# Kernel optimization log

Measured on AMD Instinct MI355X. Metric: run time of the kernel, lower is better.

## Reference

```python
import jax, jax.numpy as jnp
import numpy as np

B, C, H, W = 2, 96, 128, 128
G, NH, KH, KW = 12, 12, 3, 3
K = KH * KW
Cg = C // G          # 8 channels per deformable group
HD = C // NH         # 8 dims per head
MLP = int(2.0 * C)


def _conv3x3(x, w, b):
    y = jax.lax.conv_general_dilated(x, w, (1, 1), 'SAME',
                                     dimension_numbers=('NCHW', 'OIHW', 'NCHW'))
    return y + b[None, :, None, None]


def _prelu(x, a):
    return jnp.where(x >= 0, x, a[None, :, None, None] * x)


def _bilinear(img_flat, xs, ys, h, w):
    # img_flat: [N, C, H*W]; xs, ys: [N, P] pixel coords. Zero padding outside.
    x0 = jnp.floor(xs)
    y0 = jnp.floor(ys)
    wx = xs - x0
    wy = ys - y0

    def gather(xi, yi, wt):
        valid = ((xi >= 0) & (xi < w) & (yi >= 0) & (yi < h)).astype(img_flat.dtype)
        xc = jnp.clip(xi, 0, w - 1).astype(jnp.int32)
        yc = jnp.clip(yi, 0, h - 1).astype(jnp.int32)
        v = jnp.take_along_axis(img_flat, (yc * w + xc)[:, None, :], axis=2)
        return v * (wt * valid)[:, None, :]

    return (gather(x0, y0, (1 - wx) * (1 - wy)) + gather(x0 + 1, y0, wx * (1 - wy))
            + gather(x0, y0 + 1, (1 - wx) * wy) + gather(x0 + 1, y0 + 1, wx * wy))


def setup_inputs() -> dict:
    key = jax.random.key(0)
    ks = jax.random.split(key, 24)

    def n(k, shape, s):
        return jax.random.normal(k, shape, jnp.float32) * s

    d = {
        'feat_t': jax.random.normal(ks[0], (B, C, H, W), jnp.float32),
        'feat_kv': jax.random.normal(ks[1], (B, C, H, W), jnp.float32),
        'flow': jax.random.normal(ks[2], (B, 2, H, W), jnp.float32),
        # offset-prediction convs (zero-init in source; small random to exercise math)
        'cw1': n(ks[3], (2 * C, 2 * C + 2, 3, 3), 0.02), 'cb1': jnp.zeros((2 * C,), jnp.float32),
        'a1': jnp.full((2 * C,), 0.25, jnp.float32),
        'cw2': n(ks[4], (C, 2 * C, 3, 3), 0.02), 'cb2': jnp.zeros((C,), jnp.float32),
        'a2': jnp.full((C,), 0.25, jnp.float32),
        'cw3': n(ks[5], (G * K * 2, C, 3, 3), 0.01), 'cb3': jnp.zeros((G * K * 2,), jnp.float32),
        # attention projections
        'wq': n(ks[6], (C, C), C ** -0.5), 'bq': jnp.zeros((C,), jnp.float32),
        'wk': n(ks[7], (C, C), C ** -0.5), 'bk': jnp.zeros((C,), jnp.float32),
        'wv': n(ks[8], (C, C), C ** -0.5), 'bv': jnp.zeros((C,), jnp.float32),
        'wo': n(ks[9], (C, C), C ** -0.5), 'bo': jnp.zeros((C,), jnp.float32),
        # MLP (mlp_ratio = 2.0)
        'wm1': n(ks[10], (MLP, C), C ** -0.5), 'bm1': jnp.zeros((MLP,), jnp.float32),
        'wm2': n(ks[11], (C, MLP), MLP ** -0.5), 'bm2': jnp.zeros((C,), jnp.float32),
    }
    return d


def reference(feat_t, feat_kv, flow, cw1, cb1, a1, cw2, cb2, a2, cw3, cb3,
              wq, bq, wk, bk, wv, bv, wo, bo, wm1, bm1, wm2, bm2):
    b, c, h, w = feat_t.shape
    P = h * w
    dt = feat_t.dtype
    gy, gx = jnp.meshgrid(jnp.arange(h, dtype=dt), jnp.arange(w, dtype=dt), indexing='ij')

    # 1) backward-warp kv features to the query frame (flow channels = (x, y))
    xs = (gx[None] + flow[:, 0]).reshape(b, P)
    ys = (gy[None] + flow[:, 1]).reshape(b, P)
    kv_to_q = _bilinear(feat_kv.reshape(b, c, P), xs, ys, h, w).reshape(b, c, h, w)

    # 2) residual offsets from conv stack; add flow (flipped to (y, x)) tiled G*K times
    r = _prelu(_conv3x3(jnp.concatenate([feat_t, kv_to_q, flow], axis=1), cw1, cb1), a1)
    r = _prelu(_conv3x3(r, cw2, cb2), a2)
    r = _conv3x3(r, cw3, cb3)                                  # [B, G*K*2, H, W]
    offset = r + jnp.tile(flow[:, ::-1], (1, G * K, 1, 1))
    off = offset.reshape(b, G, K, 2, h, w)                     # [..., (dy, dx), H, W]

    # 3) grouped deformable bilinear sampling over the 3x3 window
    wy_, wx_ = jnp.meshgrid(jnp.arange(KH, dtype=dt) - (KH - 1) / 2,
                            jnp.arange(KW, dtype=dt) - (KW - 1) / 2, indexing='ij')
    win_y = wy_.reshape(K)
    win_x = wx_.reshape(K)
    sx = gx[None, None, None] + win_x[None, None, :, None, None] + off[:, :, :, 1]
    sy = gy[None, None, None] + win_y[None, None, :, None, None] + off[:, :, :, 0]
    img_g = feat_kv.reshape(b * G, Cg, P)
    samp = _bilinear(img_g, sx.reshape(b * G, K * P), sy.reshape(b * G, K * P), h, w)
    kv = samp.reshape(b, G, Cg, K, h, w).reshape(b, c, K, h, w)  # [B, C, K, H, W]

    # 4) multi-head attention: each query pixel attends over its K sampled points
    q = jnp.einsum('oc,bchw->bohw', wq, feat_t) + bq[None, :, None, None]
    k = jnp.einsum('oc,bckhw->bokhw', wk, kv) + bk[None, :, None, None, None]
    v = jnp.einsum('oc,bckhw->bokhw', wv, kv) + bv[None, :, None, None, None]
    qh = q.reshape(b, NH, HD, P)
    kh = k.reshape(b, NH, HD, K, P)
    vh = v.reshape(b, NH, HD, K, P)
    scale = 1.0 / np.sqrt(HD).astype(np.float32)
    attn = jax.nn.softmax(jnp.einsum('bhdp,bhdkp->bhkp', qh, kh) * scale, axis=2)
    o = jnp.einsum('bhkp,bhdkp->bhdp', attn, vh).reshape(b, c, h, w)
    x = feat_t + jnp.einsum('oc,bchw->bohw', wo, o) + bo[None, :, None, None]

    # 5) MLP (ratio 2.0) with residual
    hdn = jax.nn.gelu(jnp.einsum('oc,bchw->bohw', wm1, x) + bm1[None, :, None, None])
    return x + jnp.einsum('oc,bchw->bohw', wm2, hdn) + bm2[None, :, None, None]
```

## Files before the change

### kernel.cpp

```cpp
#include <hip/hip_runtime.h>
#include <hip/hip_bf16.h>
#include <math.h>

typedef __hip_bfloat16 bf16;
typedef __attribute__((ext_vector_type(8))) short s16x8;
typedef __attribute__((ext_vector_type(4))) short s16x4;
typedef __attribute__((ext_vector_type(4))) float fx4;
typedef __attribute__((ext_vector_type(2))) float f32x2;

#define Bv 2
#define Cv 96
#define Hv 128
#define Wv 128
#define Pv (Hv*Wv)
#define NPIX (Bv*Pv)
#define Gv 12
#define Kv 9
#define PPB 7
#define NPT 64
#define SROW 104
#define KROW 200

__device__ __forceinline__ float b2f(bf16 x) { return __bfloat162float(x); }
__device__ __forceinline__ bf16 f2b(float x) { return __float2bfloat16(x); }

__device__ __forceinline__ void gld16(const void* g, void* l) {
    __builtin_amdgcn_global_load_lds(
        (const __attribute__((address_space(1))) unsigned int*)g,
        (__attribute__((address_space(3))) unsigned int*)l, 16, 0, 0);
}

__device__ __forceinline__ float ldin(const void* p, size_t i, int isf) {
    return isf ? ((const float*)p)[i] : __bfloat162float(((const bf16*)p)[i]);
}

__device__ __forceinline__ void acc_pk(f32x2 acc[4], uint4 d, float wt) {
    f32x2 w2; w2.x = wt; w2.y = wt;
    #pragma unroll
    for (int q = 0; q < 4; q++) {
        unsigned u = (&d.x)[q];
        f32x2 v;
        v.x = __uint_as_float(u << 16);
        v.y = __uint_as_float(u & 0xffff0000u);
        acc[q] += w2 * v;
    }
}

__device__ __forceinline__ s16x8 pack8(const f32x2 a[4]) {
    s16x8 st;
    #pragma unroll
    for (int q = 0; q < 4; q++) {
        bf16 l = f2b(a[q].x), h = f2b(a[q].y);
        st[q*2]   = *(short*)&l;
        st[q*2+1] = *(short*)&h;
    }
    return st;
}

__global__ void detect_dtype(const unsigned short* __restrict__ x, int* __restrict__ flag,
                             float* __restrict__ zbuf)
{
    __shared__ int bad;
    if (threadIdx.x == 0) bad = 0;
    if (threadIdx.x < 64) zbuf[threadIdx.x] = 0.f;
    __syncthreads();
    int cnt = 0;
    for (int i = threadIdx.x; i < 32768; i += 256) {
        unsigned short u = x[i];
        if ((u & 0x7F80) == 0x7F80) cnt++;
    }
    atomicAdd(&bad, cnt);
    __syncthreads();
    if (threadIdx.x == 0) flag[0] = (bad > 0) ? 1 : 0;
}

__global__ void transpose_feats(const int* __restrict__ flag,
                                const void* ft, const void* fkv,
                                bf16* __restrict__ cat, bf16* __restrict__ fkvclb)
{
    __shared__ short tft[64*104];
    __shared__ short tkv[64*104];
    int tid = threadIdx.x;
    int isf = flag[0];
    int gp0 = blockIdx.x * 64;
    int bb  = gp0 >> 14;
    int p0  = gp0 & (Pv-1);

    for (int e = tid; e < 96*64; e += 256) {
        int c = e >> 6, dp = e & 63;
        size_t gi = ((size_t)bb*96 + c)*Pv + p0 + dp;
        bf16 v1 = f2b(ldin(ft,  gi, isf));
        bf16 v2 = f2b(ldin(fkv, gi, isf));
        tft[dp*104 + c] = *(short*)&v1;
        tkv[dp*104 + c] = *(short*)&v2;
    }
    __syncthreads();

    for (int u = tid; u < 64*12; u += 256) {
        int g = u % 12, px = u / 12;
        s16x8 a = *(const s16x8*)&tft[px*104 + g*8];
        s16x8 b = *(const s16x8*)&tkv[px*104 + g*8];
        *(s16x8*)(cat    + (size_t)(gp0+px)*224 + g*8) = a;
        *(s16x8*)(fkvclb + (size_t)(gp0+px)*96  + g*8) = b;
    }
}

__global__ void prep_weights(const int* __restrict__ flag,
    const void* flow,
    const void* cw1, const void* cb1, const void* a1,
    const void* cw2, const void* cb2, const void* a2,
    const void* cw3, const void* cb3,
    const void* wq, const void* bq, const void* wk, const void* bk,
    const void* wv, const void* bv, const void* wo, const void* bo,
    const void* wm1, const void* bm1, const void* wm2, const void* bm2,
    float* __restrict__ flowf,
    bf16* __restrict__ wAq, bf16* __restrict__ wAo, bf16* __restrict__ wAkv,
    bf16* __restrict__ wA1, bf16* __restrict__ wA2, bf16* __restrict__ wA3,
    bf16* __restrict__ wAm1, bf16* __restrict__ wAm2,
    float* __restrict__ biasf)
{
    int isf = flag[0];
    size_t i = (size_t)blockIdx.x * 256 + threadIdx.x;
    if (i < (size_t)Bv*2*Pv) flowf[i] = ldin(flow, i, isf);

    if (i < 9*7*192*32) {
        int q = (int)(i & 31);
        int rest = (int)(i >> 5);
        int co = rest % 192; rest /= 192;
        int kc = rest % 7;   int t = rest / 7;
        int ci = kc*32 + q;
        float v = (ci < 194) ? ldin(cw1, (size_t)co*194*9 + (size_t)ci*9 + t, isf) : 0.f;
        wA1[i] = f2b(v);
    }
    if (i < 9*6*96*32) {
        int q = (int)(i & 31);
        int rest = (int)(i >> 5);
        int co = rest % 96; rest /= 96;
        int kc = rest % 6;  int t = rest / 6;
        int ci = kc*32 + q;
        wA2[i] = f2b(ldin(cw2, (size_t)co*192*9 + (size_t)ci*9 + t, isf));
    }
    if (i < 9*3*256*32) {
        int q = (int)(i & 31);
        int rest = (int)(i >> 5);
        int co = rest % 256; rest /= 256;
        int kc = rest % 3;   int t = rest / 3;
        int ci = kc*32 + q;
        float v = (co < 216) ? ldin(cw3, (size_t)co*96*9 + (size_t)ci*9 + t, isf) : 0.f;
        wA3[i] = f2b(v);
    }
    if (i < 3*192*32) {
        int q = (int)(i & 31);
        int rest = (int)(i >> 5);
        int co = rest % 192;
        int kc = rest / 192;
        wAm1[i] = f2b(ldin(wm1, (size_t)co*96 + kc*32 + q, isf));
    }
    if (i < 6*96*32) {
        int q = (int)(i & 31);
        int rest = (int)(i >> 5);
        int co = rest % 96;
        int kc = rest / 96;
        wAm2[i] = f2b(ldin(wm2, (size_t)co*192 + kc*32 + q, isf));
    }
    if (i < 3*96*32) {
        int q = (int)(i & 31);
        int rest = (int)(i >> 5);
        int co = rest % 96;
        int kc = rest / 96;
        wAq[i] = f2b(ldin(wq, (size_t)co*96 + kc*32 + q, isf));
        wAo[i] = f2b(ldin(wo, (size_t)co*96 + kc*32 + q, isf));
    }
    if (i < 3*192*32) {
        int q = (int)(i & 31);
        int rest = (int)(i >> 5);
        int co = rest % 192;
        int kc = rest / 192;
        int ci = kc*32 + q;
        float v = (co < 96) ? ldin(wk, (size_t)co*96 + ci, isf)
                            : ldin(wv, (size_t)(co-96)*96 + ci, isf);
        wAkv[i] = f2b(v);
    }
    if (i < 192) biasf[i]       = ldin(cb1, i, isf);
    if (i < 192) biasf[192+i]   = ldin(a1, i, isf);
    if (i < 96)  biasf[384+i]   = ldin(cb2, i, isf);
    if (i < 96)  biasf[480+i]   = ldin(a2, i, isf);
    if (i < 216) biasf[576+i]   = ldin(cb3, i, isf);
    if (i < 96) {
        biasf[792+i]  = ldin(bq, i, isf);
        biasf[888+i]  = ldin(bk, i, isf);
        biasf[984+i]  = ldin(bv, i, isf);
        biasf[1080+i] = ldin(bo, i, isf);
        biasf[1368+i] = ldin(bm2, i, isf);
    }
    if (i < 192) biasf[1176+i] = ldin(bm1, i, isf);
}

__global__ void build_cat(const bf16* __restrict__ fkvclb,
                          const float* __restrict__ flowf, bf16* __restrict__ cat)
{
    int idx = blockIdx.x * 256 + threadIdx.x;
    if (idx >= NPIX*16) return;
    int grp = 12 + (idx & 15);
    int gp  = idx >> 4;
    int p   = gp & (Pv-1);
    int bb  = gp >> 14;
    s16x8 st;
    if (grp < 24) {
        int g = grp - 12;
        int py = p >> 7, px = p & (Wv-1);
        float xs = (float)px + flowf[((size_t)bb*2 + 0)*Pv + p];
        float ys = (float)py + flowf[((size_t)bb*2 + 1)*Pv + p];
        float x0f = floorf(xs), y0f = floorf(ys);
        float wx = xs - x0f, wy = ys - y0f;
        int x0 = (int)x0f, y0 = (int)y0f;
        const bf16* base = fkvclb + ((size_t)bb*Pv)*96 + g*8;
        float w[4]; uint4 t4[4];
        #pragma unroll
        for (int t = 0; t < 4; t++) {
            int xi = x0 + (t & 1), yi = y0 + (t >> 1);
            float wt = ((t & 1) ? wx : 1.f - wx) * ((t >> 1) ? wy : 1.f - wy);
            bool vld = (xi >= 0) & (xi < Wv) & (yi >= 0) & (yi < Hv);
            int xc = min(max(xi, 0), Wv-1), yc = min(max(yi, 0), Hv-1);
            w[t] = vld ? wt : 0.f;
            t4[t] = *(const uint4*)(base + (size_t)(yc*Wv + xc)*96);
        }
        f32x2 acc[4];
        #pragma unroll
        for (int q = 0; q < 4; q++) { acc[q].x = 0.f; acc[q].y = 0.f; }
        #pragma unroll
        for (int t = 0; t < 4; t++) acc_pk(acc, t4[t], w[t]);
        st = pack8(acc);
    } else if (grp == 24) {
        float fx = flowf[((size_t)bb*2 + 0)*Pv + p];
        float fy = flowf[((size_t)bb*2 + 1)*Pv + p];
        bf16 b0 = f2b(fx), b1 = f2b(fy);
        st[0] = *(short*)&b0; st[1] = *(short*)&b1;
        #pragma unroll
        for (int j = 2; j < 8; j++) st[j] = 0;
    } else {
        #pragma unroll
        for (int j = 0; j < 8; j++) st[j] = 0;
    }
    *(s16x8*)(cat + (size_t)gp*224 + grp*8) = st;
}

template<int CSTR, int CIN_PAD, int COTOT, int COF, int TAPS, int MODE, int OCS, int GY>
__launch_bounds__(256)
__global__ void conv_mfma(const bf16* __restrict__ in, const bf16* __restrict__ wA,
                          const float* __restrict__ bias, const float* __restrict__ alpha,
                          const float* __restrict__ zbuf, const int* __restrict__ flag,
                          void* __restrict__ outp, void* __restrict__ out2)
{
    constexpr int NC = CIN_PAD / 32;
    constexpr int LDS_PX = (TAPS == 9) ? 3*130 : 128;
    constexpr int NITEMS = LDS_PX * 4;
    constexpr int NSTG = (NITEMS + 255) / 256;
    constexpr int NWCH  = TAPS * COF * 64;
    constexpr int NWSTG = (NWCH + 255) / 256;
    __shared__ __align__(16) short sbuf[LDS_PX * 32];
    __shared__ __align__(16) short wlds[TAPS * COF * 512];

    int tid = threadIdx.x;
    int wave = tid >> 6, lane = tid & 63;
    int n = lane & 15, kq = lane >> 4;

    int bid = blockIdx.x;
    int xcd = bid & 7, idx = bid >> 3;
    int y   = xcd * 16 + (idx & 15);
    int cob = ((idx >> 4) % GY) * (COF*16);
    int bb  = idx / (16*GY);

    auto stage_in = [&](int kc) {
        #pragma unroll
        for (int s = 0; s < NSTG; s++) {
            int i = s*256 + tid;
            if (i < NITEMS) {
                int pxr = i >> 2;
                int kqs = i & 3;
                int part = kqs ^ ((pxr >> 1) & 3);
                const bf16* ap;
                if (TAPS == 9) {
                    int r = pxr / 130; int px = pxr - r*130;
                    int yy = y + r - 1, xx = px - 1;
                    bool inb = (yy >= 0) & (yy < Hv) & (xx >= 0) & (xx < Wv);
                    ap = inb ? (in + ((size_t)(bb*Pv + yy*Wv + xx)*CSTR + kc*32 + part*8))
                             : (const bf16*)zbuf;
                } else {
                    ap = in + ((size_t)(bb*Pv + y*Wv + pxr)*CSTR + kc*32 + part*8);
                }
                gld16(ap, &sbuf[(size_t)(i & ~63) * 8]);
            }
        }
    };
    auto stage_w = [&](int kc) {
        #pragma unroll
        for (int s = 0; s < NWSTG; s++) {
            int i = s*256 + tid;
            if (i < NWCH) {
                int t = i / (COF*64);
                int rem = i - t*(COF*64);
                int row = rem >> 2, kqs = rem & 3;
                int part = kqs ^ ((row >> 1) & 3);
                const bf16* ap = wA + ((size_t)((t*NC + kc)*COTOT + cob + row))*32 + part*8;
                gld16(ap, &wlds[(size_t)(i & ~63) * 8]);
            }
        }
    };

    fx4 acc[COF][2];
    #pragma unroll
    for (int f = 0; f < COF; f++)
        #pragma unroll
        for (int j = 0; j < 2; j++)
            acc[f][j] = (fx4){0.f, 0.f, 0.f, 0.f};

    int kqsw = kq ^ ((n >> 1) & 3);

    for (int kc = 0; kc < NC; kc++) {
        stage_in(kc); stage_w(kc);
        __syncthreads();
        #pragma unroll
        for (int t = 0; t < TAPS; t++) {
            s16x8 wf[COF];
            #pragma unroll
            for (int f = 0; f < COF; f++)
                wf[f] = *(const s16x8*)&wlds[(size_t)(((t*COF + f)*16 + n)*4 + kqsw) * 8];
            #pragma unroll
            for (int j = 0; j < 2; j++) {
                int pxs;
                if (TAPS == 9) {
                    int r = t / 3, dx = t % 3;
                    pxs = r*130 + wave*32 + j*16 + n + dx;
                } else {
                    pxs = wave*32 + j*16 + n;
                }
                int kqi = kq ^ ((pxs >> 1) & 3);
                s16x8 bfr = *(const s16x8*)&sbuf[(size_t)(pxs*4 + kqi) * 8];
                #pragma unroll
                for (int f = 0; f < COF; f++)
                    acc[f][j] = __builtin_amdgcn_mfma_f32_16x16x32_bf16(wf[f], bfr, acc[f][j], 0, 0, 0);
            }
        }
        __syncthreads();
    }

    int pxbase = wave*32;
    #pragma unroll
    for (int f = 0; f < COF; f++) {
        int co0 = cob + f*16 + kq*4;
        if (MODE == 1 && co0 >= 216) continue;
        #pragma unroll
        for (int j = 0; j < 2; j++) {
            int px = pxbase + j*16 + n;
            size_t gp = (size_t)bb*Pv + (size_t)y*Wv + px;
            fx4 fr = acc[f][j];
            s16x4 st;
            #pragma unroll
            for (int rg = 0; rg < 4; rg++) {
                float v = fr[rg] + bias[co0 + rg];
                if (MODE == 0) { float a = alpha[co0 + rg]; v = (v >= 0.f) ? v : a*v; }
                bf16 bvv = f2b(v);
                st[rg] = *(short*)&bvv;
            }
            *(s16x4*)((bf16*)outp + gp*OCS + co0) = st;
        }
    }
    (void)flag; (void)out2;
}

__launch_bounds__(256, 4)
__global__ void dka_kernel(const float* __restrict__ flowf, const bf16* __restrict__ fkvclb,
    const bf16* __restrict__ off3, const bf16* __restrict__ q_bf,
    const bf16* __restrict__ wAkv, const float* __restrict__ bkf, const float* __restrict__ bvf,
    bf16* __restrict__ o_bf)
{
    __shared__ short smem[NPT*KROW];
    short* s_s  = smem;
    short* kv_s = smem;

    int tid = threadIdx.x;
    int pb0 = blockIdx.x * PPB;

    int pt  = tid >> 2;
    int gb  = (tid & 3) * 3;
    int pxl = pt / 9;
    int tap = pt - pxl*9;
    int gp0 = pb0 + pxl;
    bool act = (pt < 63) && (gp0 < NPIX);
    int gp = act ? gp0 : (NPIX-1);
    int bb = gp >> 14, p = gp & (Pv-1);
    int py = p >> 7, px = p & (Wv-1);
    float fx = flowf[((size_t)bb*2 + 0)*Pv + p];
    float fy = flowf[((size_t)bb*2 + 1)*Pv + p];
    float sbx = (float)(px + (tap % 3) - 1) + fx;
    float sby = (float)(py + (tap / 3) - 1) + fy;
    const bf16* kvbase = fkvclb + ((size_t)bb*Pv)*96;
    unsigned owv[3];
    #pragma unroll
    for (int r = 0; r < 3; r++)
        owv[r] = *(const unsigned*)(off3 + (size_t)gp*216 + ((gb + r)*9 + tap)*2);

    float wst[2][4]; uint4 tst[2][4];
    auto stage = [&](int r, int s) {
        unsigned ow = owv[r];
        unsigned short lo16 = (unsigned short)(ow & 0xFFFFu);
        unsigned short hi16 = (unsigned short)(ow >> 16);
        float sy = sby + b2f(*(bf16*)&lo16);
        float sx = sbx + b2f(*(bf16*)&hi16);
        float x0f = floorf(sx), y0f = floorf(sy);
        float wx1 = sx - x0f, wy1 = sy - y0f;
        float wx0 = 1.f - wx1, wy0 = 1.f - wy1;
        int ix0 = (int)x0f, iy0 = (int)y0f;
        bool vx0 = (unsigned)ix0     < (unsigned)Wv;
        bool vx1 = (unsigned)(ix0+1) < (unsigned)Wv;
        bool vy0 = (unsigned)iy0     < (unsigned)Hv;
        bool vy1 = (unsigned)(iy0+1) < (unsigned)Hv;
        float mx0 = (act && vx0) ? wx0 : 0.f;
        float mx1 = (act && vx1) ? wx1 : 0.f;
        float my0 = vy0 ? wy0 : 0.f;
        float my1 = vy1 ? wy1 : 0.f;
        wst[s][0] = mx0*my0; wst[s][1] = mx1*my0;
        wst[s][2] = mx0*my1; wst[s][3] = mx1*my1;
        int xc0 = min(max(ix0,   0), Wv-1), xc1 = min(max(ix0+1, 0), Wv-1);
        int yc0 = min(max(iy0,   0), Hv-1), yc1 = min(max(iy0+1, 0), Hv-1);
        const bf16* bg = kvbase + (gb + r)*8;
        int r0 = yc0*(Wv*96), r1 = yc1*(Wv*96);
        int c0 = xc0*96,      c1 = xc1*96;
        tst[s][0] = *(const uint4*)(bg + r0 + c0);
        tst[s][1] = *(const uint4*)(bg + r0 + c1);
        tst[s][2] = *(const uint4*)(bg + r1 + c0);
        tst[s][3] = *(const uint4*)(bg + r1 + c1);
    };
    auto emit = [&](int r, int s) {
        f32x2 acc[4];
        #pragma unroll
        for (int q = 0; q < 4; q++) { acc[q].x = 0.f; acc[q].y = 0.f; }
        #pragma unroll
        for (int t = 0; t < 4; t++) acc_pk(acc, tst[s][t], wst[s][t]);
        s16x8 st = pack8(acc);
        *(s16x8*)&s_s[pt*SROW + (gb + r)*8] = st;
    };

    stage(0, 0);
    asm volatile("" ::: "memory");
    stage(1, 1);
    asm volatile("" ::: "memory");
    emit(0, 0);
    stage(2, 0);
    asm volatile("" ::: "memory");
    emit(1, 1);
    emit(2, 0);
    __syncthreads();

    {
        int wave = tid >> 6, lane = tid & 63;
        int n = lane & 15, kq = lane >> 4;
        fx4 acc[3][4];
        #pragma unroll
        for (int mi = 0; mi < 3; mi++)
            #pragma unroll
            for (int nf = 0; nf < 4; nf++)
                acc[mi][nf] = (fx4){0.f, 0.f, 0.f, 0.f};
        #pragma unroll
        for (int kc = 0; kc < 3; kc++) {
            s16x8 b[4];
            #pragma unroll
            for (int nf = 0; nf < 4; nf++)
                b[nf] = *(const s16x8*)&s_s[(nf*16 + n)*SROW + kc*32 + kq*8];
            #pragma unroll
            for (int mi = 0; mi < 3; mi++) {
                s16x8 a = *(const s16x8*)(wAkv + ((size_t)(kc*192 + (wave*3 + mi)*16 + n))*32 + kq*8);
                #pragma unroll
                for (int nf = 0; nf < 4; nf++)
                    acc[mi][nf] = __builtin_amdgcn_mfma_f32_16x16x32_bf16(a, b[nf], acc[mi][nf], 0, 0, 0);
            }
        }
        __syncthreads();
        #pragma unroll
        for (int mi = 0; mi < 3; mi++)
            #pragma unroll
            for (int nf = 0; nf < 4; nf++) {
                s16x4 st;
                #pragma unroll
                for (int rg = 0; rg < 4; rg++) {
                    bf16 bv = f2b(acc[mi][nf][rg]);
                    st[rg] = *(short*)&bv;
                }
                *(s16x4*)&kv_s[(size_t)(nf*16 + n)*KROW + (wave*3 + mi)*16 + kq*4] = st;
            }
    }
    __syncthreads();

    {
        int u = tid;
        int pxl4 = u / 12, h = u - pxl4*12;
        int gp4 = pb0 + pxl4;
        if (u < PPB*12 && gp4 < NPIX) {
            uint4 q8 = *(const uint4*)(q_bf + (size_t)gp4*96 + h*8);
            f32x2 q2[4];
            #pragma unroll
            for (int j = 0; j < 4; j++) {
                unsigned uu = (&q8.x)[j];
                q2[j].x = __uint_as_float(uu << 16);
                q2[j].y = __uint_as_float(uu & 0xffff0000u);
            }
            const f32x2* bk2 = (const f32x2*)(bkf + h*8);
            const f32x2* bv2 = (const f32x2*)(bvf + h*8);
            f32x2 qb2; qb2.x = 0.f; qb2.y = 0.f;
            #pragma unroll
            for (int j = 0; j < 4; j++) qb2 += q2[j] * bk2[j];
            float qb = qb2.x + qb2.y;
            float lg[9];
            #pragma unroll
            for (int k = 0; k < 9; k++) {
                uint4 k8 = *(const uint4*)&kv_s[(pxl4*9 + k)*KROW + h*8];
                f32x2 s2; s2.x = 0.f; s2.y = 0.f;
                #pragma unroll
                for (int j = 0; j < 4; j++) {
                    unsigned uu = (&k8.x)[j];
                    f32x2 kv2;
                    kv2.x = __uint_as_float(uu << 16);
                    kv2.y = __uint_as_float(uu & 0xffff0000u);
                    s2 += q2[j] * kv2;
                }
                lg[k] = (s2.x + s2.y + qb) * 0.35355339059327373f;
            }
            float m = lg[0];
            #pragma unroll
            for (int k = 1; k < 9; k++) m = fmaxf(m, lg[k]);
            float sum = 0.f;
            #pragma unroll
            for (int k = 0; k < 9; k++) { lg[k] = __expf(lg[k] - m); sum += lg[k]; }
            float inv = 1.f / sum;
            f32x2 ov[4];
            #pragma unroll
            for (int j = 0; j < 4; j++) ov[j] = bv2[j];
            #pragma unroll
            for (int k = 0; k < 9; k++) {
                uint4 v8 = *(const uint4*)&kv_s[(pxl4*9 + k)*KROW + 96 + h*8];
                float pw = lg[k] * inv;
                f32x2 p2; p2.x = pw; p2.y = pw;
                #pragma unroll
                for (int j = 0; j < 4; j++) {
                    unsigned uu = (&v8.x)[j];
                    f32x2 vv;
                    vv.x = __uint_as_float(uu << 16);
                    vv.y = __uint_as_float(uu & 0xffff0000u);
                    ov[j] += p2 * vv;
                }
            }
            s16x8 st = pack8(ov);
            *(s16x8*)(o_bf + (size_t)gp4*96 + h*8) = st;
        }
    }
}

__launch_bounds__(64, 4)
__global__ void tail_kernel(const bf16* __restrict__ o_bf, const bf16* __restrict__ cat,
    const bf16* __restrict__ wAo, const bf16* __restrict__ wAm1, const bf16* __restrict__ wAm2,
    const float* __restrict__ bof, const float* __restrict__ bm1f, const float* __restrict__ bm2f,
    const int* __restrict__ flag, void* __restrict__ outp)
{
    __shared__ short o_s[16*104];
    __shared__ short x_s[16*104];
    __shared__ short h_s[16*200];
    int lane = threadIdx.x;
    int n = lane & 15, kq = lane >> 4;
    int gp0 = blockIdx.x * 16;

    for (int i = lane; i < 192; i += 64) {
        int px = (i*8)/96, c = (i*8) - ((i*8)/96)*96;
        *(uint4*)&o_s[px*104 + c] = *(const uint4*)(o_bf + (size_t)(gp0+px)*96 + c);
    }
    __syncthreads();

    int gp = gp0 + n;
    int p = gp & (Pv-1), bb = gp >> 14;

    fx4 xacc[6];
    #pragma unroll
    for (int f = 0; f < 6; f++) xacc[f] = (fx4){0.f,0.f,0.f,0.f};
    #pragma unroll
    for (int kc = 0; kc < 3; kc++) {
        s16x8 b = *(const s16x8*)&o_s[n*104 + kc*32 + kq*8];
        #pragma unroll
        for (int f = 0; f < 6; f++) {
            s16x8 a = *(const s16x8*)(wAo + ((size_t)(kc*96 + f*16 + n))*32 + kq*8);
            xacc[f] = __builtin_amdgcn_mfma_f32_16x16x32_bf16(a, b, xacc[f], 0, 0, 0);
        }
    }
    #pragma unroll
    for (int f = 0; f < 6; f++) {
        int co0 = f*16 + kq*4;
        s16x4 ft4 = *(const s16x4*)(cat + (size_t)gp*224 + co0);
        s16x4 st;
        #pragma unroll
        for (int rg = 0; rg < 4; rg++) {
            short sv = ft4[rg];
            xacc[f][rg] += bof[co0+rg] + b2f(*(bf16*)&sv);
            bf16 bv = f2b(xacc[f][rg]);
            st[rg] = *(short*)&bv;
        }
        *(s16x4*)&x_s[n*104 + co0] = st;
    }
    __syncthreads();

    fx4 hacc[12];
    #pragma unroll
    for (int f = 0; f < 12; f++) hacc[f] = (fx4){0.f,0.f,0.f,0.f};
    #pragma unroll
    for (int kc = 0; kc < 3; kc++) {
        s16x8 b = *(const s16x8*)&x_s[n*104 + kc*32 + kq*8];
        #pragma unroll
        for (int f = 0; f < 12; f++) {
            s16x8 a = *(const s16x8*)(wAm1 + ((size_t)(kc*192 + f*16 + n))*32 + kq*8);
            hacc[f] = __builtin_amdgcn_mfma_f32_16x16x32_bf16(a, b, hacc[f], 0, 0, 0);
        }
    }
    #pragma unroll
    for (int f = 0; f < 12; f++) {
        int co0 = f*16 + kq*4;
        s16x4 st;
        #pragma unroll
        for (int rg = 0; rg < 4; rg++) {
            float v = hacc[f][rg] + bm1f[co0+rg];
            float t2 = __expf(1.5957691216057308f*(v + 0.044715f*v*v*v));
            v = v * t2 / (t2 + 1.f);
            bf16 bv = f2b(v);
            st[rg] = *(short*)&bv;
        }
        *(s16x4*)&h_s[n*200 + co0] = st;
    }
    __syncthreads();

    fx4 oacc[6];
    #pragma unroll
    for (int f = 0; f < 6; f++) oacc[f] = (fx4){0.f,0.f,0.f,0.f};
    #pragma unroll
    for (int kc = 0; kc < 6; kc++) {
        s16x8 b = *(const s16x8*)&h_s[n*200 + kc*32 + kq*8];
        #pragma unroll
        for (int f = 0; f < 6; f++) {
            s16x8 a = *(const s16x8*)(wAm2 + ((size_t)(kc*96 + f*16 + n))*32 + kq*8);
            oacc[f] = __builtin_amdgcn_mfma_f32_16x16x32_bf16(a, b, oacc[f], 0, 0, 0);
        }
    }
    int isf = flag[0];
    #pragma unroll
    for (int f = 0; f < 6; f++) {
        int co0 = f*16 + kq*4;
        #pragma unroll
        for (int rg = 0; rg < 4; rg++) {
            int co = co0 + rg;
            size_t oi = ((size_t)bb*Cv + co)*Pv + p;
            float v = oacc[f][rg] + bm2f[co] + xacc[f][rg];
            if (isf) ((float*)outp)[oi] = v;
            else     ((bf16*)outp)[oi] = f2b(v);
        }
    }
}

extern "C" void kernel_launch(void* const* d_in, const int* in_sizes, int n_in,
                              void* d_out, int out_size, void* d_ws, size_t ws_size,
                              hipStream_t stream) {
    (void)in_sizes; (void)n_in; (void)out_size; (void)ws_size;

    char* w = (char*)d_ws;
    bf16*  fkvclb = (bf16*) (w + 12582912);
    float* flowf  = (float*)(w + 18874368);
    bf16*  wAkv   = (bf16*) (w + 19136512);
    bf16*  wAq    = (bf16*) (w + 19173376);
    bf16*  wAo    = (bf16*) (w + 19191808);
    bf16*  wA1    = (bf16*) (w + 19210240);
    bf16*  wA2    = (bf16*) (w + 19984384);
    bf16*  wA3    = (bf16*) (w + 20316160);
    bf16*  wAm1   = (bf16*) (w + 20758528);
    bf16*  wAm2   = (bf16*) (w + 20795392);
    float* biasf  = (float*)(w + 20832256);
    float* zbuf   = biasf + 1536;
    int*   flag   = (int*)  (w + 20840448);
    char*  regA   = w + 20840704;
    char*  regB   = w + 35520768;
    char*  regC   = w + 49676544;
    char*  regD   = w + 55968000;

    bf16*  cat   = (bf16*) regA;
    bf16*  r1b   = (bf16*) regB;
    bf16*  off3  = (bf16*) regB;
    bf16*  r2b   = (bf16*) regC;
    bf16*  q_bf  = (bf16*) regC;
    bf16*  o_bf  = (bf16*) regD;

    detect_dtype<<<1, 256, 0, stream>>>((const unsigned short*)d_in[0], flag, zbuf);

    transpose_feats<<<NPIX/64, 256, 0, stream>>>(flag, d_in[0], d_in[1], cat, fkvclb);

    prep_weights<<<1536, 256, 0, stream>>>(flag,
        d_in[2],
        d_in[3], d_in[4], d_in[5], d_in[6], d_in[7], d_in[8], d_in[9], d_in[10],
        d_in[11], d_in[12], d_in[13], d_in[14], d_in[15], d_in[16], d_in[17], d_in[18],
        d_in[19], d_in[20], d_in[21], d_in[22],
        flowf, wAq, wAo, wAkv, wA1, wA2, wA3, wAm1, wAm2, biasf);

    build_cat<<<(NPIX*16 + 255)/256, 256, 0, stream>>>(fkvclb, flowf, cat);

    conv_mfma<224, 224, 192, 3, 9, 0, 192, 4><<<1024, 256, 0, stream>>>(
        cat, wA1, biasf + 0,   biasf + 192, zbuf, flag, r1b, nullptr);
    conv_mfma<192, 192,  96, 2, 9, 0,  96, 3><<<768, 256, 0, stream>>>(
        r1b, wA2, biasf + 384, biasf + 480, zbuf, flag, r2b, nullptr);
    conv_mfma< 96,  96, 256, 4, 9, 1, 216, 4><<<1024, 256, 0, stream>>>(
        r2b, wA3, biasf + 576, nullptr,     zbuf, flag, off3, nullptr);

    conv_mfma<224,  96,  96, 2, 1, 1,  96, 3><<<768, 256, 0, stream>>>(
        cat, wAq, biasf + 792, nullptr,     zbuf, flag, q_bf, nullptr);

    dka_kernel<<<(NPIX + PPB - 1)/PPB, 256, 0, stream>>>(
        flowf, fkvclb, off3, q_bf, wAkv, biasf + 888, biasf + 984, o_bf);

    tail_kernel<<<NPIX/16, 64, 0, stream>>>(
        o_bf, cat, wAo, wAm1, wAm2,
        biasf + 1080, biasf + 1176, biasf + 1368, flag, d_out);
}
```

Baseline: 296.4 us.

## Split flow channels out of first conv into separate scalar flow-conv epilogue

The first offset-prediction conv previously ran over 224 padded input channels (192 features + 2 flow + padding). The two flow channels now go through a separate scalar 3x3 conv kernel whose result is added in the first conv's epilogue before PReLU. This lets the MFMA conv use 192 input channels and shrinks the concat buffer stride. The dka kernel also stages all three sample groups before emitting, which adds register pressure and one extra launch.

```diff
diff --git a/kernel.cpp b/kernel.cpp
--- a/kernel.cpp
+++ b/kernel.cpp
@@ -20,6 +20,7 @@
 #define NPT 64
 #define SROW 104
 #define KROW 200
+#define CATS 192
 
 __device__ __forceinline__ float b2f(bf16 x) { return __bfloat162float(x); }
 __device__ __forceinline__ bf16 f2b(float x) { return __float2bfloat16(x); }
@@ -72,6 +73,59 @@
     atomicAdd(&bad, cnt);
     __syncthreads();
     if (threadIdx.x == 0) flag[0] = (bad > 0) ? 1 : 0;
+}
+
+__global__ void flowconv(const int* __restrict__ flag,
+                         const void* flow, const void* cw1,
+                         bf16* __restrict__ fc)
+{
+    __shared__ float wfl[2][9][192];
+    __shared__ float fl[2][3][72];
+    int tid = threadIdx.x;
+    int isf = flag[0];
+    int gp0 = blockIdx.x * 64;
+    int bb  = gp0 >> 14;
+    int p0  = gp0 & (Pv-1);
+    int y   = p0 >> 7;
+    int x0  = p0 & (Wv-1);
+
+    for (int i = tid; i < 3456; i += 256) {
+        int co = i % 192;
+        int rest = i / 192;
+        int t  = rest % 9;
+        int ch = rest / 9;
+        wfl[ch][t][co] = ldin(cw1, (size_t)co*194*9 + (size_t)(192+ch)*9 + t, isf);
+    }
+    for (int i = tid; i < 2*3*66; i += 256) {
+        int ch = i / 198;
+        int rem = i - ch*198;
+        int r = rem / 66, c = rem - r*66;
+        int yy = y + r - 1, xx = x0 + c - 1;
+        bool inb = (yy >= 0) & (yy < Hv) & (xx >= 0) & (xx < Wv);
+        fl[ch][r][c] = inb ? ldin(flow, ((size_t)bb*2 + ch)*Pv + yy*Wv + xx, isf) : 0.f;
+    }
+    __syncthreads();
+
+    for (int u = tid; u < 64*24; u += 256) {
+        int px = u / 24, cog = u - (u/24)*24;
+        int co0 = cog * 8;
+        float a[8];
+        #pragma unroll
+        for (int j = 0; j < 8; j++) a[j] = 0.f;
+        #pragma unroll
+        for (int t = 0; t < 9; t++) {
+            int r = t / 3, dx = t % 3;
+            float fx_ = fl[0][r][px + dx];
+            float fy_ = fl[1][r][px + dx];
+            #pragma unroll
+            for (int j = 0; j < 8; j++)
+                a[j] += wfl[0][t][co0+j]*fx_ + wfl[1][t][co0+j]*fy_;
+        }
+        s16x8 st;
+        #pragma unroll
+        for (int j = 0; j < 8; j++) { bf16 bv = f2b(a[j]); st[j] = *(short*)&bv; }
+        *(s16x8*)(fc + (size_t)(gp0+px)*CATS + co0) = st;
+    }
 }
 
 __global__ void transpose_feats(const int* __restrict__ flag,
@@ -100,8 +154,8 @@
         int g = u % 12, px = u / 12;
         s16x8 a = *(const s16x8*)&tft[px*104 + g*8];
         s16x8 b = *(const s16x8*)&tkv[px*104 + g*8];
-        *(s16x8*)(cat    + (size_t)(gp0+px)*224 + g*8) = a;
-        *(s16x8*)(fkvclb + (size_t)(gp0+px)*96  + g*8) = b;
+        *(s16x8*)(cat    + (size_t)(gp0+px)*CATS + g*8) = a;
+        *(s16x8*)(fkvclb + (size_t)(gp0+px)*96   + g*8) = b;
     }
 }
 
@@ -123,14 +177,13 @@
     size_t i = (size_t)blockIdx.x * 256 + threadIdx.x;
     if (i < (size_t)Bv*2*Pv) flowf[i] = ldin(flow, i, isf);
 
-    if (i < 9*7*192*32) {
+    if (i < 9*6*192*32) {
         int q = (int)(i & 31);
         int rest = (int)(i >> 5);
         int co = rest % 192; rest /= 192;
-        int kc = rest % 7;   int t = rest / 7;
+        int kc = rest % 6;   int t = rest / 6;
         int ci = kc*32 + q;
-        float v = (ci < 194) ? ldin(cw1, (size_t)co*194*9 + (size_t)ci*9 + t, isf) : 0.f;
-        wA1[i] = f2b(v);
+        wA1[i] = f2b(ldin(cw1, (size_t)co*194*9 + (size_t)ci*9 + t, isf));
     }
     if (i < 9*6*96*32) {
         int q = (int)(i & 31);
@@ -200,49 +253,35 @@
                           const float* __restrict__ flowf, bf16* __restrict__ cat)
 {
     int idx = blockIdx.x * 256 + threadIdx.x;
-    if (idx >= NPIX*16) return;
-    int grp = 12 + (idx & 15);
-    int gp  = idx >> 4;
+    if (idx >= NPIX*12) return;
+    int g  = idx % 12;
+    int gp = idx / 12;
     int p   = gp & (Pv-1);
     int bb  = gp >> 14;
-    s16x8 st;
-    if (grp < 24) {
-        int g = grp - 12;
-        int py = p >> 7, px = p & (Wv-1);
-        float xs = (float)px + flowf[((size_t)bb*2 + 0)*Pv + p];
-        float ys = (float)py + flowf[((size_t)bb*2 + 1)*Pv + p];
-        float x0f = floorf(xs), y0f = floorf(ys);
-        float wx = xs - x0f, wy = ys - y0f;
-        int x0 = (int)x0f, y0 = (int)y0f;
-        const bf16* base = fkvclb + ((size_t)bb*Pv)*96 + g*8;
-        float w[4]; uint4 t4[4];
-        #pragma unroll
-        for (int t = 0; t < 4; t++) {
-            int xi = x0 + (t & 1), yi = y0 + (t >> 1);
-            float wt = ((t & 1) ? wx : 1.f - wx) * ((t >> 1) ? wy : 1.f - wy);
-            bool vld = (xi >= 0) & (xi < Wv) & (yi >= 0) & (yi < Hv);
-            int xc = min(max(xi, 0), Wv-1), yc = min(max(yi, 0), Hv-1);
-            w[t] = vld ? wt : 0.f;
-            t4[t] = *(const uint4*)(base + (size_t)(yc*Wv + xc)*96);
-        }
-        f32x2 acc[4];
-        #pragma unroll
-        for (int q = 0; q < 4; q++) { acc[q].x = 0.f; acc[q].y = 0.f; }
-        #pragma unroll
-        for (int t = 0; t < 4; t++) acc_pk(acc, t4[t], w[t]);
-        st = pack8(acc);
-    } else if (grp == 24) {
-        float fx = flowf[((size_t)bb*2 + 0)*Pv + p];
-        float fy = flowf[((size_t)bb*2 + 1)*Pv + p];
-        bf16 b0 = f2b(fx), b1 = f2b(fy);
-        st[0] = *(short*)&b0; st[1] = *(short*)&b1;
-        #pragma unroll
-        for (int j = 2; j < 8; j++) st[j] = 0;
-    } else {
-        #pragma unroll
-        for (int j = 0; j < 8; j++) st[j] = 0;
-    }
-    *(s16x8*)(cat + (size_t)gp*224 + grp*8) = st;
+    int py = p >> 7, px = p & (Wv-1);
+    float xs = (float)px + flowf[((size_t)bb*2 + 0)*Pv + p];
+    float ys = (float)py + flowf[((size_t)bb*2 + 1)*Pv + p];
+    float x0f = floorf(xs), y0f = floorf(ys);
+    float wx = xs - x0f, wy = ys - y0f;
+    int x0 = (int)x0f, y0 = (int)y0f;
+    const bf16* base = fkvclb + ((size_t)bb*Pv)*96 + g*8;
+    float w[4]; uint4 t4[4];
+    #pragma unroll
+    for (int t = 0; t < 4; t++) {
+        int xi = x0 + (t & 1), yi = y0 + (t >> 1);
+        float wt = ((t & 1) ? wx : 1.f - wx) * ((t >> 1) ? wy : 1.f - wy);
+        bool vld = (xi >= 0) & (xi < Wv) & (yi >= 0) & (yi < Hv);
+        int xc = min(max(xi, 0), Wv-1), yc = min(max(yi, 0), Hv-1);
+        w[t] = vld ? wt : 0.f;
+        t4[t] = *(const uint4*)(base + (size_t)(yc*Wv + xc)*96);
+    }
+    f32x2 acc[4];
+    #pragma unroll
+    for (int q = 0; q < 4; q++) { acc[q].x = 0.f; acc[q].y = 0.f; }
+    #pragma unroll
+    for (int t = 0; t < 4; t++) acc_pk(acc, t4[t], w[t]);
+    s16x8 st = pack8(acc);
+    *(s16x8*)(cat + (size_t)gp*CATS + (12 + g)*8) = st;
 }
 
 template<int CSTR, int CIN_PAD, int COTOT, int COF, int TAPS, int MODE, int OCS, int GY>
@@ -250,7 +289,7 @@
 __global__ void conv_mfma(const bf16* __restrict__ in, const bf16* __restrict__ wA,
                           const float* __restrict__ bias, const float* __restrict__ alpha,
                           const float* __restrict__ zbuf, const int* __restrict__ flag,
-                          void* __restrict__ outp, void* __restrict__ out2)
+                          void* __restrict__ outp, const void* __restrict__ out2)
 {
     constexpr int NC = CIN_PAD / 32;
     constexpr int LDS_PX = (TAPS == 9) ? 3*130 : 128;
@@ -345,6 +384,7 @@
         __syncthreads();
     }
 
+    const bf16* fcp = (MODE == 2) ? (const bf16*)out2 : nullptr;
     int pxbase = wave*32;
     #pragma unroll
     for (int f = 0; f < COF; f++) {
@@ -355,18 +395,21 @@
             int px = pxbase + j*16 + n;
             size_t gp = (size_t)bb*Pv + (size_t)y*Wv + px;
             fx4 fr = acc[f][j];
+            s16x4 rc;
+            if (MODE == 2) rc = *(const s16x4*)(fcp + gp*CATS + co0);
             s16x4 st;
             #pragma unroll
             for (int rg = 0; rg < 4; rg++) {
                 float v = fr[rg] + bias[co0 + rg];
-                if (MODE == 0) { float a = alpha[co0 + rg]; v = (v >= 0.f) ? v : a*v; }
+                if (MODE == 2) { short sv = rc[rg]; v += b2f(*(bf16*)&sv); }
+                if (MODE == 0 || MODE == 2) { float a = alpha[co0 + rg]; v = (v >= 0.f) ? v : a*v; }
                 bf16 bvv = f2b(v);
                 st[rg] = *(short*)&bvv;
             }
             *(s16x4*)((bf16*)outp + gp*OCS + co0) = st;
         }
     }
-    (void)flag; (void)out2;
+    (void)flag;
 }
 
 __launch_bounds__(256, 4)
@@ -401,7 +444,7 @@
     for (int r = 0; r < 3; r++)
         owv[r] = *(const unsigned*)(off3 + (size_t)gp*216 + ((gb + r)*9 + tap)*2);
 
-    float wst[2][4]; uint4 tst[2][4];
+    float wst[3][4]; uint4 tst[3][4];
     auto stage = [&](int r, int s) {
         unsigned ow = owv[r];
         unsigned short lo16 = (unsigned short)(ow & 0xFFFFu);
@@ -446,11 +489,11 @@
     asm volatile("" ::: "memory");
     stage(1, 1);
     asm volatile("" ::: "memory");
+    stage(2, 2);
+    asm volatile("" ::: "memory");
     emit(0, 0);
-    stage(2, 0);
-    asm volatile("" ::: "memory");
     emit(1, 1);
-    emit(2, 0);
+    emit(2, 2);
     __syncthreads();
 
     {
@@ -593,7 +636,7 @@
     #pragma unroll
     for (int f = 0; f < 6; f++) {
         int co0 = f*16 + kq*4;
-        s16x4 ft4 = *(const s16x4*)(cat + (size_t)gp*224 + co0);
+        s16x4 ft4 = *(const s16x4*)(cat + (size_t)gp*CATS + co0);
         s16x4 st;
         #pragma unroll
         for (int rg = 0; rg < 4; rg++) {
@@ -667,6 +710,7 @@
     (void)in_sizes; (void)n_in; (void)out_size; (void)ws_size;
 
     char* w = (char*)d_ws;
+    bf16*  fc     = (bf16*) (w + 0);
     bf16*  fkvclb = (bf16*) (w + 12582912);
     float* flowf  = (float*)(w + 18874368);
     bf16*  wAkv   = (bf16*) (w + 19136512);
@@ -694,25 +738,27 @@
 
     detect_dtype<<<1, 256, 0, stream>>>((const unsigned short*)d_in[0], flag, zbuf);
 
+    flowconv<<<NPIX/64, 256, 0, stream>>>(flag, d_in[2], d_in[3], fc);
+
     transpose_feats<<<NPIX/64, 256, 0, stream>>>(flag, d_in[0], d_in[1], cat, fkvclb);
 
-    prep_weights<<<1536, 256, 0, stream>>>(flag,
+    prep_weights<<<1296, 256, 0, stream>>>(flag,
         d_in[2],
         d_in[3], d_in[4], d_in[5], d_in[6], d_in[7], d_in[8], d_in[9], d_in[10],
         d_in[11], d_in[12], d_in[13], d_in[14], d_in[15], d_in[16], d_in[17], d_in[18],
         d_in[19], d_in[20], d_in[21], d_in[22],
         flowf, wAq, wAo, wAkv, wA1, wA2, wA3, wAm1, wAm2, biasf);
 
-    build_cat<<<(NPIX*16 + 255)/256, 256, 0, stream>>>(fkvclb, flowf, cat);
-
-    conv_mfma<224, 224, 192, 3, 9, 0, 192, 4><<<1024, 256, 0, stream>>>(
-        cat, wA1, biasf + 0,   biasf + 192, zbuf, flag, r1b, nullptr);
+    build_cat<<<(NPIX*12 + 255)/256, 256, 0, stream>>>(fkvclb, flowf, cat);
+
+    conv_mfma<CATS, 192, 192, 3, 9, 2, 192, 4><<<1024, 256, 0, stream>>>(
+        cat, wA1, biasf + 0,   biasf + 192, zbuf, flag, r1b, fc);
     conv_mfma<192, 192,  96, 2, 9, 0,  96, 3><<<768, 256, 0, stream>>>(
         r1b, wA2, biasf + 384, biasf + 480, zbuf, flag, r2b, nullptr);
     conv_mfma< 96,  96, 256, 4, 9, 1, 216, 4><<<1024, 256, 0, stream>>>(
         r2b, wA3, biasf + 576, nullptr,     zbuf, flag, off3, nullptr);
 
-    conv_mfma<224,  96,  96, 2, 1, 1,  96, 3><<<768, 256, 0, stream>>>(
+    conv_mfma<CATS,  96,  96, 2, 1, 1,  96, 3><<<768, 256, 0, stream>>>(
         cat, wAq, biasf + 792, nullptr,     zbuf, flag, q_bf, nullptr);
 
     dka_kernel<<<(NPIX + PPB - 1)/PPB, 256, 0, stream>>>(
```

After: 319.3 us. 7.7% more time.
